# Kernel optimization log

Hardware: AMD Instinct MI355X
Metric: run time of the kernel (lower is better)

Reference implementation:

```python
import jax, jax.numpy as jnp
import numpy as np

N = 10000
NEG_SLOPE = 0.2

def _glorot(key, shape):
    fan = shape[0] + shape[-1]
    return jax.random.normal(key, shape, dtype=jnp.float32) * jnp.sqrt(2.0 / fan)

def gat_conv(x, src, dst, W, a_src, a_dst, b, heads, ch, concat, n):
    # PyG GATConv: linear (no bias), per-head attention logits, softmax over
    # incoming edges of each target node, weighted scatter-sum, final bias.
    h = (x @ W).reshape(n, heads, ch)                     # [N,H,C]
    al_s = jnp.einsum('nhc,hc->nh', h, a_src)             # [N,H]
    al_d = jnp.einsum('nhc,hc->nh', h, a_dst)
    e = jax.nn.leaky_relu(al_s[src] + al_d[dst], NEG_SLOPE)  # [E,H]
    emax = jax.ops.segment_max(e, dst, num_segments=n)    # [N,H]
    emax = jnp.where(jnp.isfinite(emax), emax, 0.0)
    p = jnp.exp(e - emax[dst])
    denom = jax.ops.segment_sum(p, dst, num_segments=n)   # [N,H]
    alpha = p / (denom[dst] + 1e-16)                      # [E,H]
    out = jax.ops.segment_sum(h[src] * alpha[:, :, None], dst, num_segments=n)
    out = out.reshape(n, heads * ch) if concat else out.mean(axis=1)
    return out + b

def _with_self_loops(edge_index, n):
    loop = jnp.arange(n, dtype=edge_index.dtype)
    src = jnp.concatenate([edge_index[0], loop])
    dst = jnp.concatenate([edge_index[1], loop])
    return src, dst

def setup_inputs() -> dict:
    key = jax.random.key(0)
    ks = jax.random.split(key, 20)
    in_dim, out_dim, E = 128, 256, 160000
    x = jax.random.normal(ks[0], (N, in_dim), dtype=jnp.float32)
    edge_index = jax.random.randint(ks[1], (2, E), 0, N, dtype=jnp.int64)
    return {
        'x': x, 'edge_index': edge_index,
        # conv1: GATConv(128, 256, heads=4, concat=True)
        'W1': _glorot(ks[2], (in_dim, 4 * 256)),
        'a1s': _glorot(ks[3], (4, 256)), 'a1d': _glorot(ks[4], (4, 256)),
        'b1': jnp.zeros((1024,), jnp.float32),
        'S1w': _glorot(ks[5], (in_dim, 1024)), 'S1b': jnp.zeros((1024,), jnp.float32),
        # conv2: GATConv(1024, 256, heads=4, concat=True)
        'W2': _glorot(ks[6], (1024, 4 * 256)),
        'a2s': _glorot(ks[7], (4, 256)), 'a2d': _glorot(ks[8], (4, 256)),
        'b2': jnp.zeros((1024,), jnp.float32),
        'S2w': _glorot(ks[9], (1024, 1024)), 'S2b': jnp.zeros((1024,), jnp.float32),
        # conv3: GATConv(1024, 256, heads=6, concat=False)
        'W3': _glorot(ks[10], (1024, 6 * out_dim)),
        'a3s': _glorot(ks[11], (6, out_dim)), 'a3d': _glorot(ks[12], (6, out_dim)),
        'b3': jnp.zeros((out_dim,), jnp.float32),
        'S3w': _glorot(ks[13], (1024, out_dim)), 'S3b': jnp.zeros((out_dim,), jnp.float32),
    }

def reference(x, edge_index, W1, a1s, a1d, b1, S1w, S1b,
              W2, a2s, a2d, b2, S2w, S2b,
              W3, a3s, a3d, b3, S3w, S3b):
    src, dst = _with_self_loops(edge_index, N)
    h = jax.nn.elu(gat_conv(x, src, dst, W1, a1s, a1d, b1, 4, 256, True, N) + x @ S1w + S1b)
    h = jax.nn.elu(gat_conv(h, src, dst, W2, a2s, a2d, b2, 4, 256, True, N) + h @ S2w + S2b)
    out = gat_conv(h, src, dst, W3, a3s, a3d, b3, 6, 256, False, N) + h @ S3w + S3b
    return out
```

## Files before the change

kernel.cpp:

```cpp
#include <hip/hip_runtime.h>
#include <cfloat>
#include <cmath>
#include <cstdint>

#define NN 10000
#define EE 160000
#define ETOT 170000
#define MPAD 10112

typedef _Float16 f16;
typedef __attribute__((ext_vector_type(8))) _Float16 f16x8;
typedef __attribute__((ext_vector_type(4))) float f32x4;

__global__ __launch_bounds__(256) void count_deg_k(const int* __restrict__ ei,
                                                   int* __restrict__ deg) {
    int e = blockIdx.x * 256 + threadIdx.x;
    if (e < ETOT) {
        int dst = (e < EE) ? ei[EE + e] : (e - EE);
        atomicAdd(&deg[dst], 1);
    }
}

__global__ __launch_bounds__(256) void sc1_k(const int* __restrict__ deg,
                                             int* __restrict__ tmp,
                                             int* __restrict__ bsum) {
    __shared__ int s[256];
    int i = blockIdx.x * 256 + threadIdx.x;
    int v = (i < NN) ? deg[i] : 0;
    s[threadIdx.x] = v;
    __syncthreads();
    for (int d = 1; d < 256; d <<= 1) {
        int t = (threadIdx.x >= d) ? s[threadIdx.x - d] : 0;
        __syncthreads();
        s[threadIdx.x] += t;
        __syncthreads();
    }
    if (i < NN) tmp[i] = s[threadIdx.x];
    if (threadIdx.x == 255) bsum[blockIdx.x] = s[255];
}

__global__ __launch_bounds__(64) void sc2_k(const int* __restrict__ bsum,
                                            int* __restrict__ bbase) {
    int lane = threadIdx.x;
    int v = (lane < 40) ? bsum[lane] : 0;
    int incl = v;
    for (int d = 1; d < 64; d <<= 1) {
        int t = __shfl_up(incl, d, 64);
        if (lane >= d) incl += t;
    }
    if (lane < 40) bbase[lane] = incl - v;
}

__global__ __launch_bounds__(256) void sc3_k(const int* __restrict__ deg,
                                             const int* __restrict__ tmp,
                                             const int* __restrict__ bbase,
                                             int* __restrict__ offs,
                                             int* __restrict__ pos) {
    int i = blockIdx.x * 256 + threadIdx.x;
    if (i < NN) {
        int incl = tmp[i] + bbase[blockIdx.x];
        offs[i + 1] = incl;
        pos[i]      = incl - deg[i];
    }
    if (i == 0) offs[0] = 0;
}

__global__ __launch_bounds__(256) void scatter_k(const int* __restrict__ ei,
                                                 int* __restrict__ pos,
                                                 int* __restrict__ esrc) {
    int e = blockIdx.x * 256 + threadIdx.x;
    if (e < ETOT) {
        int dst = (e < EE) ? ei[EE + e] : (e - EE);
        int src = (e < EE) ? ei[e]      : (e - EE);
        int p = atomicAdd(&pos[dst], 1);
        esrc[p] = src;
    }
}

__device__ __forceinline__ int swz(int r, int ko) { return ko ^ ((r >> 1) & 3); }

template <bool DOELU>
__global__ __launch_bounds__(256) void convA_k(const float* __restrict__ A,
                                               f16* __restrict__ hi,
                                               f16* __restrict__ lo,
                                               int M, int K, int kshift) {
    int idx = blockIdx.x * 256 + threadIdx.x;
    int row = idx >> kshift;
    int kc  = idx & ((1 << kshift) - 1);
    float v[8];
    if (row < M) {
        const float* p = A + (size_t)row * K + kc * 8;
        float4 f0 = *(const float4*)p, f1 = *(const float4*)(p + 4);
        v[0]=f0.x; v[1]=f0.y; v[2]=f0.z; v[3]=f0.w;
        v[4]=f1.x; v[5]=f1.y; v[6]=f1.z; v[7]=f1.w;
        if (DOELU) {
#pragma unroll
            for (int i = 0; i < 8; i++) v[i] = (v[i] > 0.f) ? v[i] : expf(v[i]) - 1.f;
        }
    } else {
#pragma unroll
        for (int i = 0; i < 8; i++) v[i] = 0.f;
    }
    int mblk = row >> 7, r = row & 127;
    int kblk = kc >> 2,  ko = kc & 3;
    int KB = K >> 5;
    size_t off = ((size_t)(mblk * KB + kblk)) * 4096 + r * 32 + swz(r, ko) * 8;
    f16x8 h, l;
#pragma unroll
    for (int i = 0; i < 8; i++) {
        f16 hv = (f16)v[i];
        h[i] = hv;
        l[i] = (f16)(v[i] - (float)hv);
    }
    *(f16x8*)(hi + off) = h;
    *(f16x8*)(lo + off) = l;
}

__global__ __launch_bounds__(256) void convB_k(const float* __restrict__ B,
                                               f16* __restrict__ Bdst,
                                               int NcSrc, int colOff, int KB) {
    int n  = blockIdx.x * 256 + threadIdx.x;
    int kc = blockIdx.y;
    const float* p = B + (size_t)(kc * 8) * NcSrc + n;
    int gcol = colOff + n;
    int nblk = gcol >> 7, r = gcol & 127;
    int kblk = kc >> 2,  ko = kc & 3;
    size_t off = ((size_t)(nblk * KB + kblk)) * 4096 + r * 32 + swz(r, ko) * 8;
    f16x8 h;
#pragma unroll
    for (int i = 0; i < 8; i++) h[i] = (f16)p[(size_t)i * NcSrc];
    *(f16x8*)(Bdst + off) = h;
}

__device__ __forceinline__ void gl_lds16(const void* g, void* l) {
    __builtin_amdgcn_global_load_lds(
        (const __attribute__((address_space(1))) uint32_t*)g,
        (__attribute__((address_space(3))) uint32_t*)l, 16, 0, 0);
}

#define MMBUF 24576

__global__ __launch_bounds__(256) void mm_k(const f16* __restrict__ Ahi,
                                            const f16* __restrict__ Alo,
                                            const f16* __restrict__ Bhi,
                                            float* __restrict__ C2,
                                            f16* __restrict__ C1h,
                                            const float* __restrict__ bias1,
                                            const float* __restrict__ bias2,
                                            const float* __restrict__ a_s,
                                            const float* __restrict__ a_d,
                                            float* __restrict__ als,
                                            float* __restrict__ ald,
                                            int M, int KB, int NB1,
                                            int N1, int N2, int H) {
    __shared__ __align__(16) char lds[2 * MMBUF];
    const int tid = threadIdx.x;

    const int nwg  = gridDim.x * gridDim.y;
    const int orig = blockIdx.y * gridDim.x + blockIdx.x;
    const int q = nwg >> 3, rr = nwg & 7;
    const int xcd = orig & 7, rk = orig >> 3;
    const int lin = (xcd < rr ? xcd * (q + 1) : rr * (q + 1) + (xcd - rr) * q) + rk;
    const int mblk = lin / gridDim.x, nblk = lin % gridDim.x;

    const int lane = tid & 63, w = tid >> 6;
    const int wr = w >> 1, wc = w & 1;
    const int kg = lane >> 4, l15 = lane & 15;

    int offA[4], offB[4];
#pragma unroll
    for (int t = 0; t < 4; t++) {
        int ra = wr * 64 + t * 16 + l15;
        offA[t] = ra * 64 + swz(ra, kg) * 16;
        int rb = wc * 64 + t * 16 + l15;
        offB[t] = 16384 + rb * 64 + swz(rb, kg) * 16;
    }

    const char* gAh = (const char*)Ahi + (size_t)mblk * KB * 8192;
    const char* gAl = (const char*)Alo + (size_t)mblk * KB * 8192;
    const char* gBh = (const char*)Bhi + (size_t)nblk * KB * 8192;

    f32x4 acc[4][4];
#pragma unroll
    for (int i = 0; i < 4; i++)
#pragma unroll
        for (int j = 0; j < 4; j++) acc[i][j] = (f32x4){0.f, 0.f, 0.f, 0.f};

    const int t16 = tid * 16;
    auto stage = [&](int kb, int buf) {
        const size_t tk = (size_t)kb * 8192;
        char* l = lds + buf * MMBUF;
        gl_lds16(gAh + tk + t16,        l + t16);
        gl_lds16(gAh + tk + 4096 + t16, l + 4096 + t16);
        gl_lds16(gAl + tk + t16,        l + 8192 + t16);
        gl_lds16(gAl + tk + 4096 + t16, l + 12288 + t16);
        gl_lds16(gBh + tk + t16,        l + 16384 + t16);
        gl_lds16(gBh + tk + 4096 + t16, l + 20480 + t16);
    };

    stage(0, 0);
    __syncthreads();

    for (int kb = 0; kb < KB; kb++) {
        const int cur = kb & 1;
        if (kb + 1 < KB) stage(kb + 1, cur ^ 1);

        const char* l = lds + cur * MMBUF;
        f16x8 ah[4], al[4], b[4];
#pragma unroll
        for (int t = 0; t < 4; t++) {
            ah[t] = *(const f16x8*)(l + offA[t]);
            al[t] = *(const f16x8*)(l + 8192 + offA[t]);
            b[t]  = *(const f16x8*)(l + offB[t]);
        }
#pragma unroll
        for (int i = 0; i < 4; i++)
#pragma unroll
            for (int j = 0; j < 4; j++) {
                acc[i][j] = __builtin_amdgcn_mfma_f32_16x16x32_f16(ah[i], b[j], acc[i][j], 0, 0, 0);
                acc[i][j] = __builtin_amdgcn_mfma_f32_16x16x32_f16(al[i], b[j], acc[i][j], 0, 0, 0);
            }
        __syncthreads();
    }

    const int rowBase = mblk * 128 + wr * 64;
    const int colBase = nblk * 128 + wc * 64;
    if (nblk < NB1) {
#pragma unroll
        for (int i = 0; i < 4; i++)
#pragma unroll
            for (int j = 0; j < 4; j++) {
                int col = colBase + j * 16 + l15;
#pragma unroll
                for (int q2 = 0; q2 < 4; q2++) {
                    int row = rowBase + i * 16 + kg * 4 + q2;
                    C1h[(size_t)row * N1 + col] = (f16)acc[i][j][q2];
                }
            }
        const int head = nblk >> 1;
        const int cIn  = (nblk & 1) * 128 + wc * 64;
        float asv[4], adv[4];
#pragma unroll
        for (int j = 0; j < 4; j++) {
            asv[j] = a_s[head * 256 + cIn + j * 16 + l15];
            adv[j] = a_d[head * 256 + cIn + j * 16 + l15];
        }
#pragma unroll
        for (int i = 0; i < 4; i++)
#pragma unroll
            for (int q2 = 0; q2 < 4; q2++) {
                float vs = acc[i][0][q2] * asv[0] + acc[i][1][q2] * asv[1]
                         + acc[i][2][q2] * asv[2] + acc[i][3][q2] * asv[3];
                float vd = acc[i][0][q2] * adv[0] + acc[i][1][q2] * adv[1]
                         + acc[i][2][q2] * adv[2] + acc[i][3][q2] * adv[3];
                vs += __shfl_xor(vs, 1); vs += __shfl_xor(vs, 2);
                vs += __shfl_xor(vs, 4); vs += __shfl_xor(vs, 8);
                vd += __shfl_xor(vd, 1); vd += __shfl_xor(vd, 2);
                vd += __shfl_xor(vd, 4); vd += __shfl_xor(vd, 8);
                if (l15 == 0) {
                    int row = rowBase + i * 16 + kg * 4 + q2;
                    if (row < M) {
                        atomicAdd(&als[row * H + head], vs);
                        atomicAdd(&ald[row * H + head], vd);
                    }
                }
            }
    } else {
        const int cb2 = NB1 * 128;
#pragma unroll
        for (int i = 0; i < 4; i++)
#pragma unroll
            for (int j = 0; j < 4; j++) {
                int c2 = colBase + j * 16 + l15 - cb2;
                float bsum = bias1[c2] + bias2[c2];
#pragma unroll
                for (int q2 = 0; q2 < 4; q2++) {
                    int row = rowBase + i * 16 + kg * 4 + q2;
                    if (row < M) C2[(size_t)row * N2 + c2] = acc[i][j][q2] + bsum;
                }
            }
    }
}

template <int H, bool MEAN>
__global__ __launch_bounds__(256) void smagg_k(const int* __restrict__ offs,
                                               const int* __restrict__ esrc,
                                               const float* __restrict__ als,
                                               const float* __restrict__ ald,
                                               const f16* __restrict__ hfeat16,
                                               const float* __restrict__ skipin,
                                               float* __restrict__ outf,
                                               f16* __restrict__ hiT,
                                               f16* __restrict__ loT) {
    constexpr int NC = H * 256;
    const int lane = threadIdx.x & 63;
    const int n = blockIdx.x * 4 + (threadIdx.x >> 6);
    const int base = offs[n], cnt = offs[n + 1] - base;

    float ad[H];
#pragma unroll
    for (int h = 0; h < H; h++) ad[h] = ald[n * H + h];

    float m[H], ssum[H];
#pragma unroll
    for (int h = 0; h < H; h++) { m[h] = -1e30f; ssum[h] = 0.f; }

    float acc4[16];
    float acc6[3][8];
    if (H == 4) {
#pragma unroll
        for (int i = 0; i < 16; i++) acc4[i] = 0.f;
    } else {
#pragma unroll
        for (int b = 0; b < 3; b++)
#pragma unroll
            for (int j = 0; j < 8; j++) acc6[b][j] = 0.f;
    }
    const int h0 = lane >> 4;
    const int par = (lane >= 32) ? 1 : 0;

    for (int c0 = 0; c0 < cnt; c0 += 64) {
        const int mcnt = min(64, cnt - c0);
        int src = 0;
        float l[H];
        if (lane < mcnt) {
            src = esrc[base + c0 + lane];
            if (H == 4) {
                float4 a4 = *(const float4*)(als + (size_t)src * 4);
                l[0] = a4.x + ad[0]; l[1] = a4.y + ad[1];
                l[2] = a4.z + ad[2]; l[3] = a4.w + ad[3];
            } else {
                const float2* ap = (const float2*)(als + (size_t)src * 6);
#pragma unroll
                for (int b = 0; b < 3; b++) {
                    float2 a2 = ap[b];
                    l[2 * b]     = a2.x + ad[2 * b];
                    l[2 * b + 1] = a2.y + ad[2 * b + 1];
                }
            }
#pragma unroll
            for (int h = 0; h < H; h++) l[h] = (l[h] < 0.f) ? 0.2f * l[h] : l[h];
        } else {
#pragma unroll
            for (int h = 0; h < H; h++) l[h] = -1e30f;
        }
        float sc[H], p[H];
#pragma unroll
        for (int h = 0; h < H; h++) {
            float v = l[h];
            for (int o = 32; o > 0; o >>= 1) v = fmaxf(v, __shfl_xor(v, o, 64));
            float mN = fmaxf(m[h], v);
            sc[h] = __expf(m[h] - mN);
            m[h] = mN;
            p[h] = (lane < mcnt) ? __expf(l[h] - mN) : 0.f;
            float s = p[h];
            for (int o = 32; o > 0; o >>= 1) s += __shfl_xor(s, o, 64);
            ssum[h] = ssum[h] * sc[h] + s;
        }
        if (H == 4) {
            float scm = (h0 < 2) ? ((h0 == 0) ? sc[0] : sc[1])
                                 : ((h0 == 2) ? sc[2] : sc[3]);
#pragma unroll
            for (int i = 0; i < 16; i++) acc4[i] *= scm;
        } else {
#pragma unroll
            for (int b = 0; b < 3; b++) {
                float scm = par ? sc[2 * b + 1] : sc[2 * b];
#pragma unroll
                for (int j = 0; j < 8; j++) acc6[b][j] *= scm;
            }
        }
        for (int e = 0; e < mcnt; e++) {
            int se = __shfl(src, e, 64);
            if (H == 4) {
                float pe0 = __shfl(p[0], e, 64), pe1 = __shfl(p[1], e, 64);
                float pe2 = __shfl(p[2], e, 64), pe3 = __shfl(p[3], e, 64);
                float ph = (h0 < 2) ? ((h0 == 0) ? pe0 : pe1)
                                    : ((h0 == 2) ? pe2 : pe3);
                const f16* hp = hfeat16 + (size_t)se * 1024 + lane * 16;
                f16x8 v0 = *(const f16x8*)hp;
                f16x8 v1 = *(const f16x8*)(hp + 8);
#pragma unroll
                for (int i = 0; i < 8; i++) {
                    acc4[i]     += ph * (float)v0[i];
                    acc4[8 + i] += ph * (float)v1[i];
                }
            } else {
                float pe[6];
#pragma unroll
                for (int h = 0; h < 6; h++) pe[h] = __shfl(p[h], e, 64);
                const f16* hp = hfeat16 + (size_t)se * 1536 + lane * 8;
#pragma unroll
                for (int b = 0; b < 3; b++) {
                    float ph = par ? pe[2 * b + 1] : pe[2 * b];
                    f16x8 v = *(const f16x8*)(hp + b * 512);
#pragma unroll
                    for (int j = 0; j < 8; j++) acc6[b][j] += ph * (float)v[j];
                }
            }
        }
    }

    if (MEAN) {
        float pt[8];
#pragma unroll
        for (int j = 0; j < 8; j++) pt[j] = 0.f;
#pragma unroll
        for (int b = 0; b < 3; b++) {
            float inv = 1.f / (ssum[par ? 2 * b + 1 : 2 * b] + 1e-16f);
#pragma unroll
            for (int j = 0; j < 8; j++) pt[j] += acc6[b][j] * inv;
        }
#pragma unroll
        for (int j = 0; j < 8; j++) pt[j] += __shfl_xor(pt[j], 32, 64);
        if (lane < 32) {
            float* op = outf + (size_t)n * 256 + lane * 8;
            float4 o0 = *(float4*)op, o1 = *(float4*)(op + 4);
            o0.x += pt[0] * (1.f / 6.f); o0.y += pt[1] * (1.f / 6.f);
            o0.z += pt[2] * (1.f / 6.f); o0.w += pt[3] * (1.f / 6.f);
            o1.x += pt[4] * (1.f / 6.f); o1.y += pt[5] * (1.f / 6.f);
            o1.z += pt[6] * (1.f / 6.f); o1.w += pt[7] * (1.f / 6.f);
            *(float4*)op = o0; *(float4*)(op + 4) = o1;
        }
    } else {
        float inv = 1.f / (ssum[(h0 < 2) ? ((h0 == 0) ? 0 : 1)
                                         : ((h0 == 2) ? 2 : 3)] + 1e-16f);
        const float* sp = skipin + (size_t)n * 1024 + lane * 16;
        float v[16];
#pragma unroll
        for (int c = 0; c < 4; c++) {
            float4 sk = *(const float4*)(sp + c * 4);
            v[c * 4 + 0] = sk.x + acc4[c * 4 + 0] * inv;
            v[c * 4 + 1] = sk.y + acc4[c * 4 + 1] * inv;
            v[c * 4 + 2] = sk.z + acc4[c * 4 + 2] * inv;
            v[c * 4 + 3] = sk.w + acc4[c * 4 + 3] * inv;
        }
        f16x8 hv0, lv0, hv1, lv1;
#pragma unroll
        for (int i = 0; i < 8; i++) {
            float e0 = (v[i] > 0.f) ? v[i] : expf(v[i]) - 1.f;
            float e1 = (v[8 + i] > 0.f) ? v[8 + i] : expf(v[8 + i]) - 1.f;
            f16 h0f = (f16)e0, h1f = (f16)e1;
            hv0[i] = h0f; lv0[i] = (f16)(e0 - (float)h0f);
            hv1[i] = h1f; lv1[i] = (f16)(e1 - (float)h1f);
        }
        const int mblk = n >> 7, r = n & 127;
        const int kblk = lane >> 1, ko0 = (lane & 1) * 2;
        size_t tb = ((size_t)(mblk * 32 + kblk)) * 4096 + r * 32;
        size_t off0 = tb + swz(r, ko0) * 8;
        size_t off1 = tb + swz(r, ko0 + 1) * 8;
        *(f16x8*)(hiT + off0) = hv0;
        *(f16x8*)(hiT + off1) = hv1;
        *(f16x8*)(loT + off0) = lv0;
        *(f16x8*)(loT + off1) = lv1;
    }
}

extern "C" void kernel_launch(void* const* d_in, const int* in_sizes, int n_in,
                              void* d_out, int out_size, void* d_ws, size_t ws_size,
                              hipStream_t stream) {
    const float* x   = (const float*)d_in[0];
    const int*   ei  = (const int*)d_in[1];
    const float* W1  = (const float*)d_in[2];
    const float* a1s = (const float*)d_in[3];
    const float* a1d = (const float*)d_in[4];
    const float* b1  = (const float*)d_in[5];
    const float* S1w = (const float*)d_in[6];
    const float* S1b = (const float*)d_in[7];
    const float* W2  = (const float*)d_in[8];
    const float* a2s = (const float*)d_in[9];
    const float* a2d = (const float*)d_in[10];
    const float* b2  = (const float*)d_in[11];
    const float* S2w = (const float*)d_in[12];
    const float* S2b = (const float*)d_in[13];
    const float* W3  = (const float*)d_in[14];
    const float* a3s = (const float*)d_in[15];
    const float* a3d = (const float*)d_in[16];
    const float* b3  = (const float*)d_in[17];
    const float* S3w = (const float*)d_in[18];
    const float* S3b = (const float*)d_in[19];
    float* out = (float*)d_out;

    float* ws = (float*)d_ws;
    size_t o = 0;
    float* bufA = ws + o; o += (size_t)NN * 1024;
    float* bufB = ws + o; o += (size_t)NN * 1024;
    float* als  = ws + o; o += (size_t)NN * 6;
    float* ald  = ws + o; o += (size_t)NN * 6;
    f16* hfeat16 = (f16*)(ws + o); o += (size_t)MPAD * 1536 / 2;
    f16* AhiT = (f16*)(ws + o); o += (size_t)MPAD * 1024 / 2;
    f16* AloT = (f16*)(ws + o); o += (size_t)MPAD * 1024 / 2;
    f16* Bt1  = (f16*)(ws + o); o += (size_t)16 * 4  * 4096 / 2;
    f16* Bt2  = (f16*)(ws + o); o += (size_t)16 * 32 * 4096 / 2;
    f16* Bt3  = (f16*)(ws + o); o += (size_t)14 * 32 * 4096 / 2;
    int* deg   = (int*)(ws + o);
    int* tmp   = deg + NN;
    int* bsum  = tmp + NN;
    int* bbase = bsum + 64;
    int* offs  = bbase + 64;
    int* pos   = offs + NN + 1;
    int* esrc  = pos + NN;

    hipMemsetAsync(deg, 0, NN * sizeof(int), stream);
    count_deg_k<<<(ETOT + 255) / 256, 256, 0, stream>>>(ei, deg);
    sc1_k<<<40, 256, 0, stream>>>(deg, tmp, bsum);
    sc2_k<<<1, 64, 0, stream>>>(bsum, bbase);
    sc3_k<<<40, 256, 0, stream>>>(deg, tmp, bbase, offs, pos);
    scatter_k<<<(ETOT + 255) / 256, 256, 0, stream>>>(ei, pos, esrc);

    convB_k<<<dim3(4, 16),  256, 0, stream>>>(W1,  Bt1, 1024, 0,    4);
    convB_k<<<dim3(4, 16),  256, 0, stream>>>(S1w, Bt1, 1024, 1024, 4);
    convB_k<<<dim3(4, 128), 256, 0, stream>>>(W2,  Bt2, 1024, 0,    32);
    convB_k<<<dim3(4, 128), 256, 0, stream>>>(S2w, Bt2, 1024, 1024, 32);
    convB_k<<<dim3(6, 128), 256, 0, stream>>>(W3,  Bt3, 1536, 0,    32);
    convB_k<<<dim3(1, 128), 256, 0, stream>>>(S3w, Bt3, 256,  1536, 32);

    convA_k<false><<<MPAD * 16 / 256, 256, 0, stream>>>(x, AhiT, AloT, NN, 128, 4);
    hipMemsetAsync(als, 0, NN * 12 * sizeof(float), stream);
    mm_k<<<dim3(16, 79), 256, 0, stream>>>(AhiT, AloT, Bt1, bufA, hfeat16, S1b, b1,
                                           a1s, a1d, als, ald,
                                           NN, 4, 8, 1024, 1024, 4);
    smagg_k<4, false><<<NN / 4, 256, 0, stream>>>(offs, esrc, als, ald, hfeat16,
                                                  bufA, nullptr, AhiT, AloT);

    hipMemsetAsync(als, 0, NN * 12 * sizeof(float), stream);
    mm_k<<<dim3(16, 79), 256, 0, stream>>>(AhiT, AloT, Bt2, bufB, hfeat16, S2b, b2,
                                           a2s, a2d, als, ald,
                                           NN, 32, 8, 1024, 1024, 4);
    smagg_k<4, false><<<NN / 4, 256, 0, stream>>>(offs, esrc, als, ald, hfeat16,
                                                  bufB, nullptr, AhiT, AloT);

    hipMemsetAsync(als, 0, NN * 12 * sizeof(float), stream);
    mm_k<<<dim3(14, 79), 256, 0, stream>>>(AhiT, AloT, Bt3, out, hfeat16, S3b, b3,
                                           a3s, a3d, als, ald,
                                           NN, 32, 12, 1536, 256, 6);
    smagg_k<6, true><<<NN / 4, 256, 0, stream>>>(offs, esrc, als, ald, hfeat16,
                                                 nullptr, out, nullptr, nullptr);
}
```

Measured before the change: 561.5 us.

## Batch weight conversions, fold memsets into kernels, use 8-wave GEMM blocks

Merges the six weight-conversion launches into one kernel. Removes the per-layer memsets of the attention-logit buffers by zeroing them inside convA and smagg, using ping-pong buffers and a fixed stride of 6. Moves the GEMM to 512 threads, with each wave owning 32 rows instead of 64 and the staging split across more threads. This cuts launch overhead and per-wave register pressure, at the cost of more B-fragment LDS reads per MFMA.

New measurement: 545.6 us. 1.03x faster.

```diff
diff --git a/kernel.cpp b/kernel.cpp
--- a/kernel.cpp
+++ b/kernel.cpp
@@ -79,12 +79,15 @@
 
 __device__ __forceinline__ int swz(int r, int ko) { return ko ^ ((r >> 1) & 3); }
 
-template <bool DOELU>
 __global__ __launch_bounds__(256) void convA_k(const float* __restrict__ A,
                                                f16* __restrict__ hi,
                                                f16* __restrict__ lo,
+                                               float* __restrict__ z1,
+                                               float* __restrict__ z2,
                                                int M, int K, int kshift) {
     int idx = blockIdx.x * 256 + threadIdx.x;
+    if (idx < NN * 6) z1[idx] = 0.f;
+    else if (idx < NN * 12) z2[idx - NN * 6] = 0.f;
     int row = idx >> kshift;
     int kc  = idx & ((1 << kshift) - 1);
     float v[8];
@@ -93,10 +96,6 @@
         float4 f0 = *(const float4*)p, f1 = *(const float4*)(p + 4);
         v[0]=f0.x; v[1]=f0.y; v[2]=f0.z; v[3]=f0.w;
         v[4]=f1.x; v[5]=f1.y; v[6]=f1.z; v[7]=f1.w;
-        if (DOELU) {
-#pragma unroll
-            for (int i = 0; i < 8; i++) v[i] = (v[i] > 0.f) ? v[i] : expf(v[i]) - 1.f;
-        }
     } else {
 #pragma unroll
         for (int i = 0; i < 8; i++) v[i] = 0.f;
@@ -116,11 +115,25 @@
     *(f16x8*)(lo + off) = l;
 }
 
-__global__ __launch_bounds__(256) void convB_k(const float* __restrict__ B,
-                                               f16* __restrict__ Bdst,
-                                               int NcSrc, int colOff, int KB) {
-    int n  = blockIdx.x * 256 + threadIdx.x;
-    int kc = blockIdx.y;
+__global__ __launch_bounds__(256) void convB_all_k(const float* __restrict__ W1,
+                                                   const float* __restrict__ S1w,
+                                                   const float* __restrict__ W2,
+                                                   const float* __restrict__ S2w,
+                                                   const float* __restrict__ W3,
+                                                   const float* __restrict__ S3w,
+                                                   f16* __restrict__ Bt1,
+                                                   f16* __restrict__ Bt2,
+                                                   f16* __restrict__ Bt3) {
+    int bid = blockIdx.x;
+    const float* B; f16* Bdst; int NcSrc, colOff, KB, nbx, sbid;
+    if (bid < 64)        { B = W1;  Bdst = Bt1; NcSrc = 1024; colOff = 0;    KB = 4;  nbx = 4; sbid = bid; }
+    else if (bid < 128)  { B = S1w; Bdst = Bt1; NcSrc = 1024; colOff = 1024; KB = 4;  nbx = 4; sbid = bid - 64; }
+    else if (bid < 640)  { B = W2;  Bdst = Bt2; NcSrc = 1024; colOff = 0;    KB = 32; nbx = 4; sbid = bid - 128; }
+    else if (bid < 1152) { B = S2w; Bdst = Bt2; NcSrc = 1024; colOff = 1024; KB = 32; nbx = 4; sbid = bid - 640; }
+    else if (bid < 1920) { B = W3;  Bdst = Bt3; NcSrc = 1536; colOff = 0;    KB = 32; nbx = 6; sbid = bid - 1152; }
+    else                 { B = S3w; Bdst = Bt3; NcSrc = 256;  colOff = 1536; KB = 32; nbx = 1; sbid = bid - 1920; }
+    int bx = sbid % nbx, kc = sbid / nbx;
+    int n = bx * 256 + threadIdx.x;
     const float* p = B + (size_t)(kc * 8) * NcSrc + n;
     int gcol = colOff + n;
     int nblk = gcol >> 7, r = gcol & 127;
@@ -140,7 +153,7 @@
 
 #define MMBUF 24576
 
-__global__ __launch_bounds__(256) void mm_k(const f16* __restrict__ Ahi,
+__global__ __launch_bounds__(512) void mm_k(const f16* __restrict__ Ahi,
                                             const f16* __restrict__ Alo,
                                             const f16* __restrict__ Bhi,
                                             float* __restrict__ C2,
@@ -152,7 +165,7 @@
                                             float* __restrict__ als,
                                             float* __restrict__ ald,
                                             int M, int KB, int NB1,
-                                            int N1, int N2, int H) {
+                                            int N1, int N2) {
     __shared__ __align__(16) char lds[2 * MMBUF];
     const int tid = threadIdx.x;
 
@@ -167,11 +180,14 @@
     const int wr = w >> 1, wc = w & 1;
     const int kg = lane >> 4, l15 = lane & 15;
 
-    int offA[4], offB[4];
+    int offA[2], offB[4];
+#pragma unroll
+    for (int t = 0; t < 2; t++) {
+        int ra = wr * 32 + t * 16 + l15;
+        offA[t] = ra * 64 + swz(ra, kg) * 16;
+    }
 #pragma unroll
     for (int t = 0; t < 4; t++) {
-        int ra = wr * 64 + t * 16 + l15;
-        offA[t] = ra * 64 + swz(ra, kg) * 16;
         int rb = wc * 64 + t * 16 + l15;
         offB[t] = 16384 + rb * 64 + swz(rb, kg) * 16;
     }
@@ -180,9 +196,9 @@
     const char* gAl = (const char*)Alo + (size_t)mblk * KB * 8192;
     const char* gBh = (const char*)Bhi + (size_t)nblk * KB * 8192;
 
-    f32x4 acc[4][4];
-#pragma unroll
-    for (int i = 0; i < 4; i++)
+    f32x4 acc[2][4];
+#pragma unroll
+    for (int i = 0; i < 2; i++)
 #pragma unroll
         for (int j = 0; j < 4; j++) acc[i][j] = (f32x4){0.f, 0.f, 0.f, 0.f};
 
@@ -190,12 +206,9 @@
     auto stage = [&](int kb, int buf) {
         const size_t tk = (size_t)kb * 8192;
         char* l = lds + buf * MMBUF;
-        gl_lds16(gAh + tk + t16,        l + t16);
-        gl_lds16(gAh + tk + 4096 + t16, l + 4096 + t16);
-        gl_lds16(gAl + tk + t16,        l + 8192 + t16);
-        gl_lds16(gAl + tk + 4096 + t16, l + 12288 + t16);
-        gl_lds16(gBh + tk + t16,        l + 16384 + t16);
-        gl_lds16(gBh + tk + 4096 + t16, l + 20480 + t16);
+        gl_lds16(gAh + tk + t16, l + t16);
+        gl_lds16(gAl + tk + t16, l + 8192 + t16);
+        gl_lds16(gBh + tk + t16, l + 16384 + t16);
     };
 
     stage(0, 0);
@@ -206,15 +219,16 @@
         if (kb + 1 < KB) stage(kb + 1, cur ^ 1);
 
         const char* l = lds + cur * MMBUF;
-        f16x8 ah[4], al[4], b[4];
-#pragma unroll
-        for (int t = 0; t < 4; t++) {
+        f16x8 ah[2], al[2], b[4];
+#pragma unroll
+        for (int t = 0; t < 2; t++) {
             ah[t] = *(const f16x8*)(l + offA[t]);
             al[t] = *(const f16x8*)(l + 8192 + offA[t]);
-            b[t]  = *(const f16x8*)(l + offB[t]);
-        }
-#pragma unroll
-        for (int i = 0; i < 4; i++)
+        }
+#pragma unroll
+        for (int t = 0; t < 4; t++) b[t] = *(const f16x8*)(l + offB[t]);
+#pragma unroll
+        for (int i = 0; i < 2; i++)
 #pragma unroll
             for (int j = 0; j < 4; j++) {
                 acc[i][j] = __builtin_amdgcn_mfma_f32_16x16x32_f16(ah[i], b[j], acc[i][j], 0, 0, 0);
@@ -223,11 +237,11 @@
         __syncthreads();
     }
 
-    const int rowBase = mblk * 128 + wr * 64;
+    const int rowBase = mblk * 128 + wr * 32;
     const int colBase = nblk * 128 + wc * 64;
     if (nblk < NB1) {
 #pragma unroll
-        for (int i = 0; i < 4; i++)
+        for (int i = 0; i < 2; i++)
 #pragma unroll
             for (int j = 0; j < 4; j++) {
                 int col = colBase + j * 16 + l15;
@@ -246,7 +260,7 @@
             adv[j] = a_d[head * 256 + cIn + j * 16 + l15];
         }
 #pragma unroll
-        for (int i = 0; i < 4; i++)
+        for (int i = 0; i < 2; i++)
 #pragma unroll
             for (int q2 = 0; q2 < 4; q2++) {
                 float vs = acc[i][0][q2] * asv[0] + acc[i][1][q2] * asv[1]
@@ -260,15 +274,15 @@
                 if (l15 == 0) {
                     int row = rowBase + i * 16 + kg * 4 + q2;
                     if (row < M) {
-                        atomicAdd(&als[row * H + head], vs);
-                        atomicAdd(&ald[row * H + head], vd);
+                        atomicAdd(&als[row * 6 + head], vs);
+                        atomicAdd(&ald[row * 6 + head], vd);
                     }
                 }
             }
     } else {
         const int cb2 = NB1 * 128;
 #pragma unroll
-        for (int i = 0; i < 4; i++)
+        for (int i = 0; i < 2; i++)
 #pragma unroll
             for (int j = 0; j < 4; j++) {
                 int c2 = colBase + j * 16 + l15 - cb2;
@@ -287,19 +301,25 @@
                                                const int* __restrict__ esrc,
                                                const float* __restrict__ als,
                                                const float* __restrict__ ald,
+                                               float* __restrict__ alsN,
+                                               float* __restrict__ aldN,
                                                const f16* __restrict__ hfeat16,
                                                const float* __restrict__ skipin,
                                                float* __restrict__ outf,
                                                f16* __restrict__ hiT,
                                                f16* __restrict__ loT) {
-    constexpr int NC = H * 256;
     const int lane = threadIdx.x & 63;
     const int n = blockIdx.x * 4 + (threadIdx.x >> 6);
     const int base = offs[n], cnt = offs[n + 1] - base;
 
+    if (alsN) {
+        if (lane < 6) alsN[n * 6 + lane] = 0.f;
+        else if (lane < 12) aldN[n * 6 + lane - 6] = 0.f;
+    }
+
     float ad[H];
 #pragma unroll
-    for (int h = 0; h < H; h++) ad[h] = ald[n * H + h];
+    for (int h = 0; h < H; h++) ad[h] = ald[n * 6 + h];
 
     float m[H], ssum[H];
 #pragma unroll
@@ -325,12 +345,12 @@
         float l[H];
         if (lane < mcnt) {
             src = esrc[base + c0 + lane];
+            const float2* ap = (const float2*)(als + (size_t)src * 6);
             if (H == 4) {
-                float4 a4 = *(const float4*)(als + (size_t)src * 4);
-                l[0] = a4.x + ad[0]; l[1] = a4.y + ad[1];
-                l[2] = a4.z + ad[2]; l[3] = a4.w + ad[3];
+                float2 a01 = ap[0], a23 = ap[1];
+                l[0] = a01.x + ad[0]; l[1] = a01.y + ad[1];
+                l[2] = a23.x + ad[2]; l[3] = a23.y + ad[3];
             } else {
-                const float2* ap = (const float2*)(als + (size_t)src * 6);
 #pragma unroll
                 for (int b = 0; b < 3; b++) {
                     float2 a2 = ap[b];
@@ -485,8 +505,10 @@
     size_t o = 0;
     float* bufA = ws + o; o += (size_t)NN * 1024;
     float* bufB = ws + o; o += (size_t)NN * 1024;
-    float* als  = ws + o; o += (size_t)NN * 6;
-    float* ald  = ws + o; o += (size_t)NN * 6;
+    float* als0 = ws + o; o += (size_t)NN * 6;
+    float* ald0 = ws + o; o += (size_t)NN * 6;
+    float* als1 = ws + o; o += (size_t)NN * 6;
+    float* ald1 = ws + o; o += (size_t)NN * 6;
     f16* hfeat16 = (f16*)(ws + o); o += (size_t)MPAD * 1536 / 2;
     f16* AhiT = (f16*)(ws + o); o += (size_t)MPAD * 1024 / 2;
     f16* AloT = (f16*)(ws + o); o += (size_t)MPAD * 1024 / 2;
@@ -508,32 +530,21 @@
     sc3_k<<<40, 256, 0, stream>>>(deg, tmp, bbase, offs, pos);
     scatter_k<<<(ETOT + 255) / 256, 256, 0, stream>>>(ei, pos, esrc);
 
-    convB_k<<<dim3(4, 16),  256, 0, stream>>>(W1,  Bt1, 1024, 0,    4);
-    convB_k<<<dim3(4, 16),  256, 0, stream>>>(S1w, Bt1, 1024, 1024, 4);
-    convB_k<<<dim3(4, 128), 256, 0, stream>>>(W2,  Bt2, 1024, 0,    32);
-    convB_k<<<dim3(4, 128), 256, 0, stream>>>(S2w, Bt2, 1024, 1024, 32);
-    convB_k<<<dim3(6, 128), 256, 0, stream>>>(W3,  Bt3, 1536, 0,    32);
-    convB_k<<<dim3(1, 128), 256, 0, stream>>>(S3w, Bt3, 256,  1536, 32);
-
-    convA_k<false><<<MPAD * 16 / 256, 256, 0, stream>>>(x, AhiT, AloT, NN, 128, 4);
-    hipMemsetAsync(als, 0, NN * 12 * sizeof(float), stream);
-    mm_k<<<dim3(16, 79), 256, 0, stream>>>(AhiT, AloT, Bt1, bufA, hfeat16, S1b, b1,
-                                           a1s, a1d, als, ald,
-                                           NN, 4, 8, 1024, 1024, 4);
-    smagg_k<4, false><<<NN / 4, 256, 0, stream>>>(offs, esrc, als, ald, hfeat16,
-                                                  bufA, nullptr, AhiT, AloT);
-
-    hipMemsetAsync(als, 0, NN * 12 * sizeof(float), stream);
-    mm_k<<<dim3(16, 79), 256, 0, stream>>>(AhiT, AloT, Bt2, bufB, hfeat16, S2b, b2,
-                                           a2s, a2d, als, ald,
-                                           NN, 32, 8, 1024, 1024, 4);
-    smagg_k<4, false><<<NN / 4, 256, 0, stream>>>(offs, esrc, als, ald, hfeat16,
-                                                  bufB, nullptr, AhiT, AloT);
-
-    hipMemsetAsync(als, 0, NN * 12 * sizeof(float), stream);
-    mm_k<<<dim3(14, 79), 256, 0, stream>>>(AhiT, AloT, Bt3, out, hfeat16, S3b, b3,
-                                           a3s, a3d, als, ald,
-                                           NN, 32, 12, 1536, 256, 6);
-    smagg_k<6, true><<<NN / 4, 256, 0, stream>>>(offs, esrc, als, ald, hfeat16,
-                                                 nullptr, out, nullptr, nullptr);
-}
+    convB_all_k<<<2048, 256, 0, stream>>>(W1, S1w, W2, S2w, W3, S3w, Bt1, Bt2, Bt3);
+
+    convA_k<<<MPAD * 16 / 256, 256, 0, stream>>>(x, AhiT, AloT, als0, ald0, NN, 128, 4);
+    mm_k<<<dim3(16, 79), 512, 0, stream>>>(AhiT, AloT, Bt1, bufA, hfeat16, S1b, b1,
+                                           a1s, a1d, als0, ald0, NN, 4, 8, 1024, 1024);
+    smagg_k<4, false><<<NN / 4, 256, 0, stream>>>(offs, esrc, als0, ald0, als1, ald1,
+                                                  hfeat16, bufA, nullptr, AhiT, AloT);
+
+    mm_k<<<dim3(16, 79), 512, 0, stream>>>(AhiT, AloT, Bt2, bufB, hfeat16, S2b, b2,
+                                           a2s, a2d, als1, ald1, NN, 32, 8, 1024, 1024);
+    smagg_k<4, false><<<NN / 4, 256, 0, stream>>>(offs, esrc, als1, ald1, als0, ald0,
+                                                  hfeat16, bufB, nullptr, AhiT, AloT);
+
+    mm_k<<<dim3(14, 79), 512, 0, stream>>>(AhiT, AloT, Bt3, out, hfeat16, S3b, b3,
+                                           a3s, a3d, als0, ald0, NN, 32, 12, 1536, 256);
+    smagg_k<6, true><<<NN / 4, 256, 0, stream>>>(offs, esrc, als0, ald0, nullptr, nullptr,
+                                                 hfeat16, nullptr, out, nullptr, nullptr);
+}
```
